# Optimization experiments

Hardware: AMD Instinct MI355X
Metric: run time of the kernel (lower is better)

The kernel has to match this reference:

```python
import jax, jax.numpy as jnp
import numpy as np

B, T, E, UNITS = 64, 256, 1024, 1024

def hard_sigmoid(x):
    # Keras K.hard_sigmoid: clip(0.2*x + 0.5, 0, 1)
    return jnp.clip(0.2 * x + 0.5, 0.0, 1.0)

def setup_inputs() -> dict:
    key = jax.random.key(0)
    ks = jax.random.split(key, 11)
    d = {
        "all_inputs": jax.random.normal(ks[0], (B, T, E + UNITS), dtype=jnp.float32),
        "h0": jnp.zeros((B, UNITS), dtype=jnp.float32),
    }
    names = ["W_r", "U_r", "C_r", "W_z", "U_z", "C_z", "W", "U", "C"]
    shapes = {"W_r": (UNITS, UNITS), "U_r": (UNITS, UNITS), "C_r": (E, UNITS),
              "W_z": (UNITS, UNITS), "U_z": (UNITS, UNITS), "C_z": (E, UNITS),
              "W": (UNITS, UNITS), "U": (UNITS, UNITS), "C": (E, UNITS)}
    for i, n in enumerate(names):
        d[n] = jax.random.uniform(ks[i + 2], shapes[n], dtype=jnp.float32,
                                  minval=-0.05, maxval=0.05)
    return d

def reference(all_inputs, h0, W_r, U_r, C_r, W_z, U_z, C_z, W, U, C):
    enc = C_r.shape[0]  # encoder_size
    xs = jnp.swapaxes(all_inputs, 0, 1)  # [T, B, E+units]

    def step(h, x):
        ctx = x[:, :enc]       # encoder context
        emb = x[:, enc:]       # decoder embedding input
        r = hard_sigmoid(emb @ W_r + h @ U_r + ctx @ C_r)
        z = hard_sigmoid(emb @ W_z + h @ U_z + ctx @ C_z)
        h_cand = jnp.tanh(emb @ W + (h * r) @ U + ctx @ C)
        h_new = (1.0 - z) * h + z * h_cand
        return h_new, h_new

    _, ys = jax.lax.scan(step, h0, xs)  # ys: [T, B, units]
    return jnp.swapaxes(ys, 0, 1)       # [B, T, units]
```

## Files before the change

### kernel.cpp

```cpp
#include <hip/hip_runtime.h>
#include <hip/hip_bf16.h>
#include <stdint.h>

#define B_   64
#define T_   256
#define KIN  2048
#define N3   3072
#define M_   16384
#define RBLK 256
#define RTHR 256

typedef __attribute__((ext_vector_type(8))) short short8;
typedef __attribute__((ext_vector_type(4))) float f32x4;
typedef unsigned long long u64;

static __device__ __forceinline__ float bf2f(short s) {
    union { float f; uint32_t u; } c; c.u = ((uint32_t)(uint16_t)s) << 16; return c.f;
}
static __device__ __forceinline__ float u16tof(uint32_t u) {
    union { float f; uint32_t x; } c; c.x = u << 16; return c.f;
}
static __device__ __forceinline__ short f2bf(float f) {
    union { float f; uint32_t u; } c; c.f = f;
    uint32_t u = c.u;
    uint32_t r = (u + 0x7fffu + ((u >> 16) & 1u)) >> 16;
    return (short)(uint16_t)r;
}

#define CLDC(dst, ptr) asm volatile("global_load_dwordx4 %0, %1, off sc0 sc1" : "=v"(dst) : "v"(ptr))
#define CLDU16(dst, ptr) asm volatile("global_load_ushort %0, %1, off"        : "=v"(dst) : "v"(ptr))
static __device__ __forceinline__ void cst8(void* p, u64 v) {
    asm volatile("global_store_dwordx2 %0, %1, off sc0 sc1" :: "v"(p), "v"(v) : "memory");
}

__global__ __launch_bounds__(256)
void k_prep_w(const float* __restrict__ Wr, const float* __restrict__ Ur, const float* __restrict__ Cr,
              const float* __restrict__ Wz, const float* __restrict__ Uz, const float* __restrict__ Cz,
              const float* __restrict__ Wc, const float* __restrict__ Uc, const float* __restrict__ Cc,
              short* __restrict__ WcatT, short* __restrict__ UcatT, short* __restrict__ UcT)
{
    __shared__ float tile[32][33];
    int m = blockIdx.z;
    const float* src; short* dst; int ld, noff, koff;
    switch (m) {
      case 0: src=Cr; dst=WcatT; ld=KIN;  noff=0;    koff=0;    break;
      case 1: src=Wr; dst=WcatT; ld=KIN;  noff=0;    koff=1024; break;
      case 2: src=Cz; dst=WcatT; ld=KIN;  noff=1024; koff=0;    break;
      case 3: src=Wz; dst=WcatT; ld=KIN;  noff=1024; koff=1024; break;
      case 4: src=Cc; dst=WcatT; ld=KIN;  noff=2048; koff=0;    break;
      case 5: src=Wc; dst=WcatT; ld=KIN;  noff=2048; koff=1024; break;
      case 6: src=Ur; dst=UcatT; ld=1024; noff=0;    koff=0;    break;
      case 7: src=Uz; dst=UcatT; ld=1024; noff=1024; koff=0;    break;
      default: src=Uc; dst=UcT;  ld=1024; noff=0;    koff=0;    break;
    }
    int n0 = blockIdx.x * 32, k0 = blockIdx.y * 32;
    int tx = threadIdx.x, ty = threadIdx.y;
    #pragma unroll
    for (int i = 0; i < 32; i += 8)
        tile[ty + i][tx] = src[(long)(k0 + ty + i) * 1024 + (n0 + tx)];
    __syncthreads();
    #pragma unroll
    for (int i = 0; i < 32; i += 8)
        dst[(long)(noff + n0 + ty + i) * ld + koff + k0 + tx] = f2bf(tile[tx][ty + i]);
}

__global__ __launch_bounds__(256)
void k_prep_x(const float* __restrict__ X, short* __restrict__ Xb, long n8)
{
    long i = (long)blockIdx.x * blockDim.x + threadIdx.x;
    long stride = (long)gridDim.x * blockDim.x;
    for (; i < n8; i += stride) {
        const float4* p = (const float4*)(X + i * 8);
        float4 a = p[0], b = p[1];
        short8 o;
        o[0]=f2bf(a.x); o[1]=f2bf(a.y); o[2]=f2bf(a.z); o[3]=f2bf(a.w);
        o[4]=f2bf(b.x); o[5]=f2bf(b.y); o[6]=f2bf(b.z); o[7]=f2bf(b.w);
        *(short8*)(Xb + i * 8) = o;
    }
}

__global__ __launch_bounds__(256)
void k_init_h(const float* __restrict__ h0, float* __restrict__ h,
              short* __restrict__ hbRM, short* __restrict__ hbF,
              uint32_t* __restrict__ flags)
{
    int i = blockIdx.x * 256 + threadIdx.x;
    float v = h0[i];
    h[i] = v;
    short bv = f2bf(v);
    hbRM[i] = bv;
    int b = i >> 10, k = i & 1023;
    int bg = b >> 4, row = b & 15, kk = k >> 5, ksub = (k & 31) >> 3, e = k & 7;
    hbF[bg * 16384 + kk * 512 + row * 32 + ksub * 8 + e] = bv;
    if (i < 8192) flags[i] = 0;
}

__global__ __launch_bounds__(256)
void k_gemm_x(const short* __restrict__ Xb, const short* __restrict__ WcatT, short* __restrict__ P)
{
    __shared__ short As[128 * 64];
    __shared__ short Bs[128 * 64];
    int tid = threadIdx.x;
    int lane = tid & 63, wave = tid >> 6;
    int i0 = blockIdx.y * 128;
    int n0 = blockIdx.x * 128;
    int wrow = (wave >> 1) * 64, wcol = (wave & 1) * 64;
    f32x4 acc[4][4] = {};

    for (int k0 = 0; k0 < KIN; k0 += 64) {
        __syncthreads();
        #pragma unroll
        for (int j = 0; j < 4; j++) {
            int e = (j * 256 + tid) * 8;
            int row = e >> 6, k = e & 63;
            short8 va = *(const short8*)(Xb    + (long)(i0 + row) * KIN + k0 + k);
            short8 vb = *(const short8*)(WcatT + (long)(n0 + row) * KIN + k0 + k);
            int byt = row * 128 + ((k * 2) ^ ((row & 7) << 4));
            *(short8*)((char*)As + byt) = va;
            *(short8*)((char*)Bs + byt) = vb;
        }
        __syncthreads();
        #pragma unroll
        for (int kk = 0; kk < 64; kk += 32) {
            short8 af[4], bfr[4];
            int kel = kk + (lane >> 4) * 8;
            #pragma unroll
            for (int rt = 0; rt < 4; rt++) {
                int row = wrow + rt * 16 + (lane & 15);
                int byt = row * 128 + ((kel * 2) ^ ((row & 7) << 4));
                af[rt] = *(const short8*)((const char*)As + byt);
            }
            #pragma unroll
            for (int ct = 0; ct < 4; ct++) {
                int row = wcol + ct * 16 + (lane & 15);
                int byt = row * 128 + ((kel * 2) ^ ((row & 7) << 4));
                bfr[ct] = *(const short8*)((const char*)Bs + byt);
            }
            #pragma unroll
            for (int rt = 0; rt < 4; rt++)
                #pragma unroll
                for (int ct = 0; ct < 4; ct++)
                    acc[rt][ct] = __builtin_amdgcn_mfma_f32_16x16x32_bf16(af[rt], bfr[ct], acc[rt][ct], 0, 0, 0);
        }
    }
    #pragma unroll
    for (int rt = 0; rt < 4; rt++)
      #pragma unroll
      for (int ct = 0; ct < 4; ct++)
        #pragma unroll
        for (int r = 0; r < 4; r++) {
            int row = i0 + wrow + rt * 16 + (lane >> 4) * 4 + r;
            int prow = ((row & 255) << 6) | (row >> 8);
            int col = n0 + wcol + ct * 16 + (lane & 15);
            P[(long)prow * N3 + col] = f2bf(acc[rt][ct][r]);
        }
}

__global__ __launch_bounds__(RTHR)
void k_recur6(const short* __restrict__ UcatT, const short* __restrict__ UcT,
              const short* __restrict__ P, const float* __restrict__ hG,
              char* __restrict__ hbF, char* __restrict__ rhF,
              uint32_t* __restrict__ flags, float* __restrict__ out)
{
    __shared__ short wbuf[49152];
    __shared__ float pbuf[1024];
    __shared__ float pbuf2[1024];
    __shared__ float h_lds[256];
    __shared__ float z_lds[256];
    __shared__ short tscr[320];

    const int tid  = threadIdx.x;
    const int lane = tid & 63, w = tid >> 6;
    const int col16 = lane & 15, rquad = (lane >> 4) * 4;
    const int bg = blockIdx.x >> 6;
    const int cg = blockIdx.x & 63;
    const int c0 = cg * 16;
    const int grpbase = bg * 64;

    #pragma unroll 4
    for (int i = 0; i < 24; i++) {
        int c = tid + i * 256;
        int tau = c >> 11, cc = c & 2047;
        int kk = cc >> 6, l = cc & 63;
        const short* srcp;
        if (tau == 0)      srcp = UcatT + (c0 + (l & 15)) * 1024 + kk * 32 + ((l >> 4) & 3) * 8;
        else if (tau == 1) srcp = UcatT + (1024 + c0 + (l & 15)) * 1024 + kk * 32 + ((l >> 4) & 3) * 8;
        else               srcp = UcT   + (c0 + (l & 15)) * 1024 + kk * 32 + ((l >> 4) & 3) * 8;
        *(short8*)((char*)wbuf + c * 16) = *(const short8*)srcp;
    }
    h_lds[tid] = hG[(bg * 16 + (tid >> 4)) * 1024 + c0 + (tid & 15)];
    __syncthreads();

    const char* aA  = hbF + bg * 32768 + (w * 8) * 1024 + (lane & 15) * 64 + (lane >> 4) * 16;
    const char* aB  = rhF + bg * 32768 + (w * 8) * 1024 + (lane & 15) * 64 + (lane >> 4) * 16;
    const char* wbR = (const char*)wbuf + (w * 8) * 1024 + lane * 16;
    const char* wbZ = (const char*)wbuf + 32768 + (w * 8) * 1024 + lane * 16;
    const char* wbC = (const char*)wbuf + 65536 + (w * 8) * 1024 + lane * 16;
    const int kkp = c0 >> 5, halfp = (c0 >> 4) & 1;
    float* mypb  = pbuf  + w * 256 + lane * 4;
    float* mypb2 = pbuf2 + w * 256 + lane * 4;

    uint32_t pr[4], pz[4], pc[4];
    {
        const char* Pb = (const char*)(P + (long)(bg * 16) * N3 + c0 + col16);
        if (w == 0) {
            #pragma unroll
            for (int r = 0; r < 4; r++) CLDU16(pr[r], Pb + (long)(rquad + r) * N3 * 2);
            #pragma unroll
            for (int r = 0; r < 4; r++) CLDU16(pc[r], Pb + ((long)(rquad + r) * N3 + 2048) * 2);
        } else if (w == 1) {
            #pragma unroll
            for (int r = 0; r < 4; r++) CLDU16(pz[r], Pb + ((long)(rquad + r) * N3 + 1024) * 2);
        }
    }

    for (int t = 0; t < T_; t++) {
        if (w == 0) {
            uint32_t tgt = 2u * t;
            for (;;) {
                uint32_t v = __hip_atomic_load(flags + (grpbase + lane) * 32,
                                               __ATOMIC_RELAXED, __HIP_MEMORY_SCOPE_AGENT);
                if (__all((int)(v >= tgt))) break;
            }
        }
        __syncthreads();

        if (t > 0)
            out[((long)(bg * 16 + (tid >> 4)) * T_ + (t - 1)) * 1024 + c0 + (tid & 15)] = h_lds[tid];

        short8 a[8];
        #pragma unroll
        for (int j = 0; j < 8; j++) CLDC(a[j], aA + j * 1024);
        asm volatile("s_waitcnt vmcnt(0)" ::: "memory");
        __builtin_amdgcn_sched_barrier(0);

        f32x4 acc = {};
        #pragma unroll
        for (int j = 0; j < 8; j++) {
            short8 bw = *(const short8*)(wbR + j * 1024);
            acc = __builtin_amdgcn_mfma_f32_16x16x32_bf16(a[j], bw, acc, 0, 0, 0);
        }
        *(f32x4*)mypb = acc;
        asm volatile("s_waitcnt lgkmcnt(0)" ::: "memory");
        __syncthreads();

        if (w == 0) {
            f32x4 s = *(const f32x4*)(pbuf + lane * 4) + *(const f32x4*)(pbuf + 256 + lane * 4)
                    + *(const f32x4*)(pbuf + 512 + lane * 4) + *(const f32x4*)(pbuf + 768 + lane * 4);
            #pragma unroll
            for (int r = 0; r < 4; r++) {
                float pre = s[r] + u16tof(pr[r]);
                float v = fminf(fmaxf(0.2f * pre + 0.5f, 0.f), 1.f);
                tscr[(rquad + r) * 20 + col16] = f2bf(v * h_lds[(rquad + r) * 16 + col16]);
            }
            asm volatile("s_waitcnt lgkmcnt(0)" ::: "memory");
            __builtin_amdgcn_sched_barrier(0);
            u64 vv = *(const u64*)((const char*)tscr + (lane & 15) * 40 + (lane >> 4) * 8);
            cst8(rhF + bg * 32768 + kkp * 1024 + (lane & 15) * 64 + halfp * 32 + (lane >> 4) * 8, vv);
            asm volatile("s_waitcnt vmcnt(0)" ::: "memory");
            if (lane == 0)
                __hip_atomic_store(flags + blockIdx.x * 32, 2u * t + 1u,
                                   __ATOMIC_RELAXED, __HIP_MEMORY_SCOPE_AGENT);
        }
        f32x4 accz = {};
        #pragma unroll
        for (int j = 0; j < 8; j++) {
            short8 bw = *(const short8*)(wbZ + j * 1024);
            accz = __builtin_amdgcn_mfma_f32_16x16x32_bf16(a[j], bw, accz, 0, 0, 0);
        }
        *(f32x4*)mypb2 = accz;
        asm volatile("s_waitcnt lgkmcnt(0)" ::: "memory");

        if (w == 0) {
            uint32_t tgt = 2u * t + 1u;
            for (;;) {
                uint32_t v = __hip_atomic_load(flags + (grpbase + lane) * 32,
                                               __ATOMIC_RELAXED, __HIP_MEMORY_SCOPE_AGENT);
                if (__all((int)(v >= tgt))) break;
            }
        }
        __syncthreads();

        #pragma unroll
        for (int j = 0; j < 8; j++) CLDC(a[j], aB + j * 1024);

        if (w == 1) {
            f32x4 sz = *(const f32x4*)(pbuf2 + lane * 4) + *(const f32x4*)(pbuf2 + 256 + lane * 4)
                     + *(const f32x4*)(pbuf2 + 512 + lane * 4) + *(const f32x4*)(pbuf2 + 768 + lane * 4);
            #pragma unroll
            for (int r = 0; r < 4; r++) {
                float pre = sz[r] + u16tof(pz[r]);
                z_lds[(rquad + r) * 16 + col16] = fminf(fmaxf(0.2f * pre + 0.5f, 0.f), 1.f);
            }
        }
        asm volatile("s_waitcnt vmcnt(0)" ::: "memory");
        __builtin_amdgcn_sched_barrier(0);

        f32x4 accc = {};
        #pragma unroll
        for (int j = 0; j < 8; j++) {
            short8 bw = *(const short8*)(wbC + j * 1024);
            accc = __builtin_amdgcn_mfma_f32_16x16x32_bf16(a[j], bw, accc, 0, 0, 0);
        }
        *(f32x4*)mypb = accc;
        asm volatile("s_waitcnt lgkmcnt(0)" ::: "memory");
        __syncthreads();

        if (w == 0) {
            f32x4 s = *(const f32x4*)(pbuf + lane * 4) + *(const f32x4*)(pbuf + 256 + lane * 4)
                    + *(const f32x4*)(pbuf + 512 + lane * 4) + *(const f32x4*)(pbuf + 768 + lane * 4);
            #pragma unroll
            for (int r = 0; r < 4; r++) {
                int idx = (rquad + r) * 16 + col16;
                float pre = s[r] + u16tof(pc[r]);
                float hc = tanhf(pre);
                float z  = z_lds[idx];
                float ho = h_lds[idx];
                float hn = (1.f - z) * ho + z * hc;
                h_lds[idx] = hn;
                tscr[(rquad + r) * 20 + col16] = f2bf(hn);
            }
            asm volatile("s_waitcnt lgkmcnt(0)" ::: "memory");
            __builtin_amdgcn_sched_barrier(0);
            u64 vv = *(const u64*)((const char*)tscr + (lane & 15) * 40 + (lane >> 4) * 8);
            cst8(hbF + bg * 32768 + kkp * 1024 + (lane & 15) * 64 + halfp * 32 + (lane >> 4) * 8, vv);
            asm volatile("s_waitcnt vmcnt(0)" ::: "memory");
            if (lane == 0)
                __hip_atomic_store(flags + blockIdx.x * 32, 2u * t + 2u,
                                   __ATOMIC_RELAXED, __HIP_MEMORY_SCOPE_AGENT);
        }

        {
            int tn = (t + 1) & 255;
            const char* Pb = (const char*)(P + ((long)tn * 64 + bg * 16) * N3 + c0 + col16);
            if (w == 0) {
                #pragma unroll
                for (int r = 0; r < 4; r++) CLDU16(pr[r], Pb + (long)(rquad + r) * N3 * 2);
                #pragma unroll
                for (int r = 0; r < 4; r++) CLDU16(pc[r], Pb + ((long)(rquad + r) * N3 + 2048) * 2);
            } else if (w == 1) {
                #pragma unroll
                for (int r = 0; r < 4; r++) CLDU16(pz[r], Pb + ((long)(rquad + r) * N3 + 1024) * 2);
            }
        }
    }

    __syncthreads();

    out[((long)(bg * 16 + (tid >> 4)) * T_ + 255) * 1024 + c0 + (tid & 15)] = h_lds[tid];
}

__global__ __launch_bounds__(256)
void k_stepA(const short* __restrict__ hb, const short* __restrict__ UcatT,
             const short* __restrict__ P, const float* __restrict__ h,
             short* __restrict__ rh, float* __restrict__ zbuf, int t)
{
    int lane = threadIdx.x & 63, wave = threadIdx.x >> 6;
    int wid = blockIdx.x * 4 + wave;
    int ct = wid & 127, rt = wid >> 7;
    int r0 = rt * 16, n0 = ct * 16;
    int lrow = lane & 15, lk = (lane >> 4) * 8;
    f32x4 acc = {0.f, 0.f, 0.f, 0.f};
    const short8* Aptr = (const short8*)(hb    + (r0 + lrow) * 1024 + lk);
    const short8* Bptr = (const short8*)(UcatT + (n0 + lrow) * 1024 + lk);
    #pragma unroll 8
    for (int kk = 0; kk < 32; kk++)
        acc = __builtin_amdgcn_mfma_f32_16x16x32_bf16(Aptr[kk * 4], Bptr[kk * 4], acc, 0, 0, 0);

    int col = n0 + (lane & 15);
    int brb = r0 + (lane >> 4) * 4;
    #pragma unroll
    for (int r = 0; r < 4; r++) {
        int b = brb + r;
        float pre = acc[r] + bf2f(P[((long)t * 64 + b) * N3 + col]);
        float v = fminf(fmaxf(0.2f * pre + 0.5f, 0.f), 1.f);
        if (col < 1024)
            rh[b * 1024 + col] = f2bf(v * h[b * 1024 + col]);
        else
            zbuf[b * 1024 + (col - 1024)] = v;
    }
}

__global__ __launch_bounds__(256)
void k_stepB(const short* __restrict__ rh, const short* __restrict__ UcT,
             const short* __restrict__ P, const float* __restrict__ zbuf,
             float* __restrict__ h, short* __restrict__ hb,
             float* __restrict__ out, int t)
{
    int lane = threadIdx.x & 63, wave = threadIdx.x >> 6;
    int wid = blockIdx.x * 4 + wave;
    int ct = wid & 63, rt = wid >> 6;
    int r0 = rt * 16, n0 = ct * 16;
    int lrow = lane & 15, lk = (lane >> 4) * 8;
    f32x4 acc = {0.f, 0.f, 0.f, 0.f};
    const short8* Aptr = (const short8*)(rh  + (r0 + lrow) * 1024 + lk);
    const short8* Bptr = (const short8*)(UcT + (n0 + lrow) * 1024 + lk);
    #pragma unroll 8
    for (int kk = 0; kk < 32; kk++)
        acc = __builtin_amdgcn_mfma_f32_16x16x32_bf16(Aptr[kk * 4], Bptr[kk * 4], acc, 0, 0, 0);

    int col = n0 + (lane & 15);
    int brb = r0 + (lane >> 4) * 4;
    #pragma unroll
    for (int r = 0; r < 4; r++) {
        int b = brb + r;
        float pre = acc[r] + bf2f(P[((long)t * 64 + b) * N3 + 2048 + col]);
        float hc = tanhf(pre);
        float z  = zbuf[b * 1024 + col];
        float ho = h[b * 1024 + col];
        float hn = (1.f - z) * ho + z * hc;
        h[b * 1024 + col]  = hn;
        hb[b * 1024 + col] = f2bf(hn);
        out[((long)b * T_ + t) * 1024 + col] = hn;
    }
}

extern "C" void kernel_launch(void* const* d_in, const int* in_sizes, int n_in,
                              void* d_out, int out_size, void* d_ws, size_t ws_size,
                              hipStream_t stream)
{
    (void)in_sizes; (void)n_in; (void)out_size; (void)ws_size;
    const float* X   = (const float*)d_in[0];
    const float* h0  = (const float*)d_in[1];
    const float* W_r = (const float*)d_in[2];
    const float* U_r = (const float*)d_in[3];
    const float* C_r = (const float*)d_in[4];
    const float* W_z = (const float*)d_in[5];
    const float* U_z = (const float*)d_in[6];
    const float* C_z = (const float*)d_in[7];
    const float* W   = (const float*)d_in[8];
    const float* U   = (const float*)d_in[9];
    const float* C   = (const float*)d_in[10];

    char* ws = (char*)d_ws;
    size_t off = 0;
    short* WcatT = (short*)(ws + off); off += (size_t)N3 * KIN * 2;
    short* UcatT = (short*)(ws + off); off += (size_t)2048 * 1024 * 2;
    short* UcT   = (short*)(ws + off); off += (size_t)1024 * 1024 * 2;
    short* Xb    = (short*)(ws + off); off += (size_t)M_ * KIN * 2;
    short* P     = (short*)(ws + off); off += (size_t)M_ * N3 * 2;
    float* h     = (float*)(ws + off); off += (size_t)B_ * 1024 * 4;
    short* hbRM  = (short*)(ws + off); off += (size_t)B_ * 1024 * 2;
    short* rhRM  = (short*)(ws + off); off += (size_t)B_ * 1024 * 2;
    float* zbuf  = (float*)(ws + off); off += (size_t)B_ * 1024 * 4;
    char*  hbF   = (char*)(ws + off);  off += (size_t)B_ * 1024 * 2;
    char*  rhF   = (char*)(ws + off);  off += (size_t)B_ * 1024 * 2;
    uint32_t* flags = (uint32_t*)(ws + off); off += 32768;

    k_prep_w<<<dim3(32, 32, 9), dim3(32, 8), 0, stream>>>(W_r, U_r, C_r, W_z, U_z, C_z, W, U, C,
                                                          WcatT, UcatT, UcT);
    k_prep_x<<<2048, 256, 0, stream>>>(X, Xb, (long)M_ * KIN / 8);
    k_init_h<<<256, 256, 0, stream>>>(h0, h, hbRM, (short*)hbF, flags);
    k_gemm_x<<<dim3(N3 / 128, M_ / 128), 256, 0, stream>>>(Xb, WcatT, P);

    float* out = (float*)d_out;
    void* args[] = { (void*)&UcatT, (void*)&UcT, (void*)&P, (void*)&h, (void*)&hbF,
                     (void*)&rhF, (void*)&flags, (void*)&out };
    hipError_t e = hipLaunchCooperativeKernel((const void*)k_recur6, dim3(RBLK), dim3(RTHR),
                                              args, 0, stream);
    if (e != hipSuccess) {
        for (int t = 0; t < T_; t++) {
            k_stepA<<<128, 256, 0, stream>>>(hbRM, UcatT, P, h, rhRM, zbuf, t);
            k_stepB<<<64, 256, 0, stream>>>(rhRM, UcT, P, zbuf, h, hbRM, out, t);
        }
    }
}
```

Baseline: 1.730 ms.

## Replace per-step block barriers with per-wave flag spins and keep h in registers

Every wave now polls the cross-block flags itself, which removes two __syncthreads per timestep. The z-gate MFMA is issued before the first barrier so both r and z partials reduce together, each with its own LDS buffer. The hidden state lives in wave-0 registers instead of LDS, and wave 0 writes the output directly. The aim is to shorten the serial critical path of each recurrence step, at the cost of more waves polling global memory.

```diff
diff --git a/kernel.cpp b/kernel.cpp
--- a/kernel.cpp
+++ b/kernel.cpp
@@ -157,15 +157,15 @@
 }
 
 __global__ __launch_bounds__(RTHR)
-void k_recur6(const short* __restrict__ UcatT, const short* __restrict__ UcT,
+void k_recur7(const short* __restrict__ UcatT, const short* __restrict__ UcT,
               const short* __restrict__ P, const float* __restrict__ hG,
               char* __restrict__ hbF, char* __restrict__ rhF,
               uint32_t* __restrict__ flags, float* __restrict__ out)
 {
     __shared__ short wbuf[49152];
-    __shared__ float pbuf[1024];
-    __shared__ float pbuf2[1024];
-    __shared__ float h_lds[256];
+    __shared__ float pbR[1024];
+    __shared__ float pbZ[1024];
+    __shared__ float pbC[1024];
     __shared__ float z_lds[256];
     __shared__ short tscr[320];
 
@@ -188,7 +188,12 @@
         else               srcp = UcT   + (c0 + (l & 15)) * 1024 + kk * 32 + ((l >> 4) & 3) * 8;
         *(short8*)((char*)wbuf + c * 16) = *(const short8*)srcp;
     }
-    h_lds[tid] = hG[(bg * 16 + (tid >> 4)) * 1024 + c0 + (tid & 15)];
+    f32x4 hreg = {};
+    if (w == 0) {
+        #pragma unroll
+        for (int r = 0; r < 4; r++)
+            hreg[r] = hG[(bg * 16 + rquad + r) * 1024 + c0 + col16];
+    }
     __syncthreads();
 
     const char* aA  = hbF + bg * 32768 + (w * 8) * 1024 + (lane & 15) * 64 + (lane >> 4) * 16;
@@ -197,8 +202,9 @@
     const char* wbZ = (const char*)wbuf + 32768 + (w * 8) * 1024 + lane * 16;
     const char* wbC = (const char*)wbuf + 65536 + (w * 8) * 1024 + lane * 16;
     const int kkp = c0 >> 5, halfp = (c0 >> 4) & 1;
-    float* mypb  = pbuf  + w * 256 + lane * 4;
-    float* mypb2 = pbuf2 + w * 256 + lane * 4;
+    float* mypbR = pbR + w * 256 + lane * 4;
+    float* mypbZ = pbZ + w * 256 + lane * 4;
+    float* mypbC = pbC + w * 256 + lane * 4;
 
     uint32_t pr[4], pz[4], pc[4];
     {
@@ -215,7 +221,7 @@
     }
 
     for (int t = 0; t < T_; t++) {
-        if (w == 0) {
+        {
             uint32_t tgt = 2u * t;
             for (;;) {
                 uint32_t v = __hip_atomic_load(flags + (grpbase + lane) * 32,
@@ -223,35 +229,37 @@
                 if (__all((int)(v >= tgt))) break;
             }
         }
-        __syncthreads();
-
-        if (t > 0)
-            out[((long)(bg * 16 + (tid >> 4)) * T_ + (t - 1)) * 1024 + c0 + (tid & 15)] = h_lds[tid];
-
         short8 a[8];
         #pragma unroll
         for (int j = 0; j < 8; j++) CLDC(a[j], aA + j * 1024);
         asm volatile("s_waitcnt vmcnt(0)" ::: "memory");
         __builtin_amdgcn_sched_barrier(0);
 
-        f32x4 acc = {};
+        f32x4 accr = {};
         #pragma unroll
         for (int j = 0; j < 8; j++) {
             short8 bw = *(const short8*)(wbR + j * 1024);
-            acc = __builtin_amdgcn_mfma_f32_16x16x32_bf16(a[j], bw, acc, 0, 0, 0);
-        }
-        *(f32x4*)mypb = acc;
+            accr = __builtin_amdgcn_mfma_f32_16x16x32_bf16(a[j], bw, accr, 0, 0, 0);
+        }
+        *(f32x4*)mypbR = accr;
+        f32x4 accz = {};
+        #pragma unroll
+        for (int j = 0; j < 8; j++) {
+            short8 bw = *(const short8*)(wbZ + j * 1024);
+            accz = __builtin_amdgcn_mfma_f32_16x16x32_bf16(a[j], bw, accz, 0, 0, 0);
+        }
+        *(f32x4*)mypbZ = accz;
         asm volatile("s_waitcnt lgkmcnt(0)" ::: "memory");
         __syncthreads();
 
         if (w == 0) {
-            f32x4 s = *(const f32x4*)(pbuf + lane * 4) + *(const f32x4*)(pbuf + 256 + lane * 4)
-                    + *(const f32x4*)(pbuf + 512 + lane * 4) + *(const f32x4*)(pbuf + 768 + lane * 4);
+            f32x4 s = *(const f32x4*)(pbR + lane * 4) + *(const f32x4*)(pbR + 256 + lane * 4)
+                    + *(const f32x4*)(pbR + 512 + lane * 4) + *(const f32x4*)(pbR + 768 + lane * 4);
             #pragma unroll
             for (int r = 0; r < 4; r++) {
                 float pre = s[r] + u16tof(pr[r]);
                 float v = fminf(fmaxf(0.2f * pre + 0.5f, 0.f), 1.f);
-                tscr[(rquad + r) * 20 + col16] = f2bf(v * h_lds[(rquad + r) * 16 + col16]);
+                tscr[(rquad + r) * 20 + col16] = f2bf(v * hreg[r]);
             }
             asm volatile("s_waitcnt lgkmcnt(0)" ::: "memory");
             __builtin_amdgcn_sched_barrier(0);
@@ -261,17 +269,17 @@
             if (lane == 0)
                 __hip_atomic_store(flags + blockIdx.x * 32, 2u * t + 1u,
                                    __ATOMIC_RELAXED, __HIP_MEMORY_SCOPE_AGENT);
-        }
-        f32x4 accz = {};
-        #pragma unroll
-        for (int j = 0; j < 8; j++) {
-            short8 bw = *(const short8*)(wbZ + j * 1024);
-            accz = __builtin_amdgcn_mfma_f32_16x16x32_bf16(a[j], bw, accz, 0, 0, 0);
-        }
-        *(f32x4*)mypb2 = accz;
-        asm volatile("s_waitcnt lgkmcnt(0)" ::: "memory");
-
-        if (w == 0) {
+        } else if (w == 1) {
+            f32x4 sz = *(const f32x4*)(pbZ + lane * 4) + *(const f32x4*)(pbZ + 256 + lane * 4)
+                     + *(const f32x4*)(pbZ + 512 + lane * 4) + *(const f32x4*)(pbZ + 768 + lane * 4);
+            #pragma unroll
+            for (int r = 0; r < 4; r++) {
+                float pre = sz[r] + u16tof(pz[r]);
+                z_lds[(rquad + r) * 16 + col16] = fminf(fmaxf(0.2f * pre + 0.5f, 0.f), 1.f);
+            }
+        }
+
+        {
             uint32_t tgt = 2u * t + 1u;
             for (;;) {
                 uint32_t v = __hip_atomic_load(flags + (grpbase + lane) * 32,
@@ -279,20 +287,8 @@
                 if (__all((int)(v >= tgt))) break;
             }
         }
-        __syncthreads();
-
         #pragma unroll
         for (int j = 0; j < 8; j++) CLDC(a[j], aB + j * 1024);
-
-        if (w == 1) {
-            f32x4 sz = *(const f32x4*)(pbuf2 + lane * 4) + *(const f32x4*)(pbuf2 + 256 + lane * 4)
-                     + *(const f32x4*)(pbuf2 + 512 + lane * 4) + *(const f32x4*)(pbuf2 + 768 + lane * 4);
-            #pragma unroll
-            for (int r = 0; r < 4; r++) {
-                float pre = sz[r] + u16tof(pz[r]);
-                z_lds[(rquad + r) * 16 + col16] = fminf(fmaxf(0.2f * pre + 0.5f, 0.f), 1.f);
-            }
-        }
         asm volatile("s_waitcnt vmcnt(0)" ::: "memory");
         __builtin_amdgcn_sched_barrier(0);
 
@@ -302,22 +298,20 @@
             short8 bw = *(const short8*)(wbC + j * 1024);
             accc = __builtin_amdgcn_mfma_f32_16x16x32_bf16(a[j], bw, accc, 0, 0, 0);
         }
-        *(f32x4*)mypb = accc;
+        *(f32x4*)mypbC = accc;
         asm volatile("s_waitcnt lgkmcnt(0)" ::: "memory");
         __syncthreads();
 
         if (w == 0) {
-            f32x4 s = *(const f32x4*)(pbuf + lane * 4) + *(const f32x4*)(pbuf + 256 + lane * 4)
-                    + *(const f32x4*)(pbuf + 512 + lane * 4) + *(const f32x4*)(pbuf + 768 + lane * 4);
+            f32x4 s = *(const f32x4*)(pbC + lane * 4) + *(const f32x4*)(pbC + 256 + lane * 4)
+                    + *(const f32x4*)(pbC + 512 + lane * 4) + *(const f32x4*)(pbC + 768 + lane * 4);
             #pragma unroll
             for (int r = 0; r < 4; r++) {
-                int idx = (rquad + r) * 16 + col16;
                 float pre = s[r] + u16tof(pc[r]);
                 float hc = tanhf(pre);
-                float z  = z_lds[idx];
-                float ho = h_lds[idx];
-                float hn = (1.f - z) * ho + z * hc;
-                h_lds[idx] = hn;
+                float z  = z_lds[(rquad + r) * 16 + col16];
+                float hn = (1.f - z) * hreg[r] + z * hc;
+                hreg[r] = hn;
                 tscr[(rquad + r) * 20 + col16] = f2bf(hn);
             }
             asm volatile("s_waitcnt lgkmcnt(0)" ::: "memory");
@@ -328,6 +322,9 @@
             if (lane == 0)
                 __hip_atomic_store(flags + blockIdx.x * 32, 2u * t + 2u,
                                    __ATOMIC_RELAXED, __HIP_MEMORY_SCOPE_AGENT);
+            #pragma unroll
+            for (int r = 0; r < 4; r++)
+                out[((long)(bg * 16 + rquad + r) * T_ + t) * 1024 + c0 + col16] = hreg[r];
         }
 
         {
@@ -344,10 +341,6 @@
             }
         }
     }
-
-    __syncthreads();
-
-    out[((long)(bg * 16 + (tid >> 4)) * T_ + 255) * 1024 + c0 + (tid & 15)] = h_lds[tid];
 }
 
 __global__ __launch_bounds__(256)
@@ -456,7 +449,7 @@
     float* out = (float*)d_out;
     void* args[] = { (void*)&UcatT, (void*)&UcT, (void*)&P, (void*)&h, (void*)&hbF,
                      (void*)&rhF, (void*)&flags, (void*)&out };
-    hipError_t e = hipLaunchCooperativeKernel((const void*)k_recur6, dim3(RBLK), dim3(RTHR),
+    hipError_t e = hipLaunchCooperativeKernel((const void*)k_recur7, dim3(RBLK), dim3(RTHR),
                                               args, 0, stream);
     if (e != hipSuccess) {
         for (int t = 0; t < T_; t++) {
```

Result: slower. 2.081 ms (+20.3%).
